# Performance work log

Measured on AMD Instinct MI355X. Metric: run time of the kernel, lower is better.

Reference implementation:

```python
import jax, jax.numpy as jnp
import numpy as np

B, S, D_IN, D_OUT = 4, 2048, 4096, 4096


def setup_inputs() -> dict:
    key = jax.random.key(0)
    k1, k2 = jax.random.split(key)
    x = jax.random.normal(k1, (B, S, D_IN), dtype=jnp.float32)
    # kaiming-uniform-like init scale; exact distribution irrelevant for correctness
    bound = 1.0 / np.sqrt(D_IN)
    weight = jax.random.uniform(k2, (D_OUT, D_IN), dtype=jnp.float32,
                                minval=-bound, maxval=bound)
    return {"x": x, "weight": weight}


def reference(x, weight):
    # absmean scale: gamma = mean(|W|)
    gamma = jnp.mean(jnp.abs(weight))
    # ternary quantize: round(W/gamma) clipped to {-1, 0, 1}; guard gamma==0
    safe_gamma = jnp.where(gamma == 0, 1.0, gamma)
    w_q = jnp.clip(jnp.round(weight / safe_gamma), -1.0, 1.0)
    w_q = jnp.where(gamma == 0, jnp.zeros_like(weight), w_q)
    # output = gamma * (x @ W_q^T)   (F.linear with no bias, scaled)
    out = jnp.einsum("bsd,od->bso", x, w_q) * gamma
    return out
```

## Files before the change

### kernel.cpp

```cpp
#include <hip/hip_runtime.h>
#include <hip/hip_bf16.h>
#include <stdint.h>

#define K_DIM 4096

typedef __attribute__((ext_vector_type(4))) float f32x4;
typedef __attribute__((ext_vector_type(4))) int i32x4;

#define GLOAD_LDS16(g, l)                                                        \
  __builtin_amdgcn_global_load_lds(                                              \
      (const __attribute__((address_space(1))) void*)(g),                        \
      (__attribute__((address_space(3))) void*)(l), 16, 0, 0)

__global__ void absum_partial(const float* __restrict__ W,
                              float* __restrict__ partials, int n) {
  int tid = blockIdx.x * blockDim.x + threadIdx.x;
  int stride = gridDim.x * blockDim.x;
  const f32x4* W4 = (const f32x4*)W;
  int n4 = n >> 2;
  float s = 0.f;
  for (int i = tid; i < n4; i += stride) {
    f32x4 v = W4[i];
    s += fabsf(v[0]) + fabsf(v[1]) + fabsf(v[2]) + fabsf(v[3]);
  }
#pragma unroll
  for (int off = 32; off > 0; off >>= 1) s += __shfl_down(s, off, 64);
  __shared__ float wsum[4];
  if ((threadIdx.x & 63) == 0) wsum[threadIdx.x >> 6] = s;
  __syncthreads();
  if (threadIdx.x == 0)
    partials[blockIdx.x] = wsum[0] + wsum[1] + wsum[2] + wsum[3];
}

__global__ void gamma_finalize(const float* __restrict__ partials,
                               float* __restrict__ gamma, float inv_n) {
  __shared__ float sm[256];
  int t = threadIdx.x;
  sm[t] = partials[t] + partials[t + 256] + partials[t + 512] + partials[t + 768];
  __syncthreads();
  for (int off = 128; off > 0; off >>= 1) {
    if (t < off) sm[t] += sm[t + off];
    __syncthreads();
  }
  if (t == 0) gamma[0] = sm[0] * inv_n;
}

__global__ void quantize_w_i8(const float* __restrict__ W,
                              signed char* __restrict__ Wq,
                              const float* __restrict__ gamma_p, int n) {
  float g = gamma_p[0];
  float safe = (g == 0.f) ? 1.f : g;
  int tid = blockIdx.x * blockDim.x + threadIdx.x;
  int stride = gridDim.x * blockDim.x;
  const f32x4* W4 = (const f32x4*)W;
  int n4 = n >> 2;
  int* out = (int*)Wq;
  for (int i = tid; i < n4; i += stride) {
    f32x4 v = W4[i];
    int b0, b1, b2, b3;
    float t0 = rintf(v[0] / safe);
    float t1 = rintf(v[1] / safe);
    float t2 = rintf(v[2] / safe);
    float t3 = rintf(v[3] / safe);
    b0 = (t0 >= 0.5f) ? 1 : (t0 <= -0.5f ? -1 : 0);
    b1 = (t1 >= 0.5f) ? 1 : (t1 <= -0.5f ? -1 : 0);
    b2 = (t2 >= 0.5f) ? 1 : (t2 <= -0.5f ? -1 : 0);
    b3 = (t3 >= 0.5f) ? 1 : (t3 <= -0.5f ? -1 : 0);
    out[i] = (b0 & 255) | ((b1 & 255) << 8) | ((b2 & 255) << 16) |
             ((b3 & 255) << 24);
  }
}

__global__ __launch_bounds__(256)
void quant_x_i8(const float* __restrict__ X, signed char* __restrict__ Xq,
                float* __restrict__ xscale) {
  int row = blockIdx.x;
  int t = threadIdx.x;
  const f32x4* xr = (const f32x4*)(X + (size_t)row * K_DIM);
  f32x4 v0 = xr[t], v1 = xr[t + 256], v2 = xr[t + 512], v3 = xr[t + 768];
  float mx = 0.f;
#define AMAX4(V)                                                               \
  mx = fmaxf(mx, fmaxf(fmaxf(fabsf(V[0]), fabsf(V[1])),                        \
                       fmaxf(fabsf(V[2]), fabsf(V[3]))));
  AMAX4(v0) AMAX4(v1) AMAX4(v2) AMAX4(v3)
#undef AMAX4
#pragma unroll
  for (int off = 32; off > 0; off >>= 1) mx = fmaxf(mx, __shfl_down(mx, off, 64));
  __shared__ float wmx[4];
  if ((t & 63) == 0) wmx[t >> 6] = mx;
  __syncthreads();
  float rmax = fmaxf(fmaxf(wmx[0], wmx[1]), fmaxf(wmx[2], wmx[3]));
  float inv = (rmax > 0.f) ? 127.0f / rmax : 0.f;
  if (t == 0) xscale[row] = (rmax > 0.f) ? rmax / 127.0f : 0.f;
  int* out = (int*)(Xq + (size_t)row * K_DIM);
#define PACK(V, IDX)                                                           \
  {                                                                            \
    int c0 = __float2int_rn(V[0] * inv), c1 = __float2int_rn(V[1] * inv);      \
    int c2 = __float2int_rn(V[2] * inv), c3 = __float2int_rn(V[3] * inv);      \
    out[IDX] = (c0 & 255) | ((c1 & 255) << 8) | ((c2 & 255) << 16) |           \
               ((c3 & 255) << 24);                                             \
  }
  PACK(v0, t) PACK(v1, t + 256) PACK(v2, t + 512) PACK(v3, t + 768)
#undef PACK
}

__global__ __launch_bounds__(512, 2)
void gemm256_i8(const signed char* __restrict__ A,
                const signed char* __restrict__ Bq,
                float* __restrict__ C,
                const float* __restrict__ gamma_p,
                const float* __restrict__ xscale, int M, int N) {
  __shared__ __align__(16) signed char Abuf[2][256][64];
  __shared__ __align__(16) signed char Bbuf[2][256][64];

  int ntN = N >> 8;
  int bid = blockIdx.x;
  int swz = (bid & 7) * (gridDim.x >> 3) + (bid >> 3);
  int tm = swz / ntN, tn = swz % ntN;

  int t = threadIdx.x;
  int lane = t & 63;
  int wid = t >> 6;
  int wr = wid >> 2, wc = wid & 3;
  int lr = lane & 15;
  int sc0 = (lane >> 4) ^ ((lr >> 1) & 3);

  const signed char* aG = A + (size_t)tm * 256 * K_DIM;
  const signed char* bG = Bq + (size_t)tn * 256 * K_DIM;

  int srow = t >> 2;
  int schunk = (t & 3) ^ ((t >> 3) & 3);
  const signed char* aSg = aG + (size_t)srow * K_DIM + (schunk << 4);
  const signed char* bSg = bG + (size_t)srow * K_DIM + (schunk << 4);
  char* aSl = (char*)Abuf + t * 16;
  char* bSl = (char*)Bbuf + t * 16;

  const signed char* aRd = &Abuf[0][0][0] + (wr * 128 + lr) * 64 + sc0 * 16;
  const signed char* bRd = &Bbuf[0][0][0] + (wc * 64 + lr) * 64 + sc0 * 16;

  i32x4 acc[8][4];
#pragma unroll
  for (int m = 0; m < 8; ++m)
#pragma unroll
    for (int n = 0; n < 4; ++n) acc[m][n] = (i32x4)(0);

#define STAGE_A(jj, S)                                                         \
  { GLOAD_LDS16(aSg + (size_t)(jj) * 64, aSl + (S) * 16384);                   \
    GLOAD_LDS16(aSg + (size_t)(jj) * 64 + (size_t)128 * K_DIM,                 \
                aSl + (S) * 16384 + 8192); }
#define STAGE_B(jj, S)                                                         \
  { GLOAD_LDS16(bSg + (size_t)(jj) * 64, bSl + (S) * 16384);                   \
    GLOAD_LDS16(bSg + (size_t)(jj) * 64 + (size_t)128 * K_DIM,                 \
                bSl + (S) * 16384 + 8192); }
#define BAR() __builtin_amdgcn_s_barrier()
#define VMC0() asm volatile("s_waitcnt vmcnt(0)" ::: "memory")
#define LGKM(NN) asm volatile("s_waitcnt lgkmcnt(" #NN ")" ::: "memory")
#define SB0() __builtin_amdgcn_sched_barrier(0)

#define TILE(S, JSTG, DO_STG, DO_END)                                          \
  {                                                                            \
    if (DO_STG) { STAGE_A(JSTG, (S) ^ 1); STAGE_B(JSTG, (S) ^ 1); }            \
    _Pragma("unroll") for (int n = 0; n < 4; ++n)                              \
      bfr[n] = *(const i32x4*)(bRd + (S) * 16384 + n * 1024);                  \
    _Pragma("unroll") for (int m = 0; m < 4; ++m)                              \
      at[m] = *(const i32x4*)(aRd + (S) * 16384 + m * 1024);                   \
    SB0();                                                                     \
    _Pragma("unroll") for (int m = 0; m < 4; ++m)                              \
      ab[m] = *(const i32x4*)(aRd + (S) * 16384 + 4096 + m * 1024);            \
    SB0();                                                                     \
    LGKM(4); SB0();                                                            \
    __builtin_amdgcn_s_setprio(1);                                             \
    _Pragma("unroll") for (int m = 0; m < 4; ++m)                              \
      _Pragma("unroll") for (int n = 0; n < 4; ++n)                            \
        acc[m][n] = __builtin_amdgcn_mfma_i32_16x16x64_i8(                     \
            at[m], bfr[n], acc[m][n], 0, 0, 0);                                \
    __builtin_amdgcn_s_setprio(0);                                             \
    LGKM(0); SB0();                                                            \
    __builtin_amdgcn_s_setprio(1);                                             \
    _Pragma("unroll") for (int m = 0; m < 4; ++m)                              \
      _Pragma("unroll") for (int n = 0; n < 4; ++n)                            \
        acc[4 + m][n] = __builtin_amdgcn_mfma_i32_16x16x64_i8(                 \
            ab[m], bfr[n], acc[4 + m][n], 0, 0, 0);                            \
    __builtin_amdgcn_s_setprio(0);                                             \
    if (DO_END) { VMC0(); BAR(); }                                             \
  }

  STAGE_A(0, 0); STAGE_B(0, 0);
  VMC0();
  BAR();

  i32x4 at[4], ab[4], bfr[4];
  for (int i = 0; i < 31; ++i) {
    int p = i << 1;
    TILE(0, p + 1, 1, 1);
    TILE(1, p + 2, 1, 1);
  }
  TILE(0, 63, 1, 1);
  TILE(1, 0, 0, 0);

  float g = gamma_p[0];
  int crow = (lane >> 4) << 2;
  size_t row0 = (size_t)tm * 256 + wr * 128 + crow;
  int col0 = tn * 256 + wc * 64 + lr;
#pragma unroll
  for (int m = 0; m < 8; ++m) {
#pragma unroll
    for (int j = 0; j < 4; ++j) {
      size_t row = row0 + m * 16 + j;
      float sc = g * xscale[row];
      float* cp = C + row * (size_t)N + col0;
#pragma unroll
      for (int n = 0; n < 4; ++n) cp[n * 16] = (float)acc[m][n][j] * sc;
    }
  }
#undef STAGE_A
#undef STAGE_B
#undef BAR
#undef VMC0
#undef LGKM
#undef SB0
#undef TILE
}

__global__ void naive_bitlinear(const float* __restrict__ X,
                                const float* __restrict__ W,
                                float* __restrict__ out,
                                const float* __restrict__ gamma_p, int M, int N) {
  int col = blockIdx.x * blockDim.x + threadIdx.x;
  int row = blockIdx.y;
  if (col >= N || row >= M) return;
  float g = gamma_p[0];
  float safe = (g == 0.f) ? 1.f : g;
  const float* x = X + (size_t)row * K_DIM;
  const float* w = W + (size_t)col * K_DIM;
  float s = 0.f;
  for (int k = 0; k < K_DIM; ++k) {
    float qv = fminf(fmaxf(rintf(w[k] / safe), -1.f), 1.f);
    s += x[k] * qv;
  }
  out[(size_t)row * N + col] = s * g;
}

extern "C" void kernel_launch(void* const* d_in, const int* in_sizes, int n_in,
                              void* d_out, int out_size, void* d_ws,
                              size_t ws_size, hipStream_t stream) {
  const float* x = (const float*)d_in[0];
  const float* w = (const float*)d_in[1];
  float* out = (float*)d_out;
  int xn = in_sizes[0];
  int wn = in_sizes[1];
  int M = xn / K_DIM;
  int N = wn / K_DIM;

  char* ws = (char*)d_ws;
  float* partials = (float*)ws;
  float* gamma = (float*)(ws + 4096);
  float* xscale = (float*)(ws + 8192);
  signed char* Wq = (signed char*)(ws + 8192 + 32768);
  signed char* Xq = Wq + (size_t)wn;
  size_t need = 8192 + 32768 + (size_t)wn + (size_t)xn;

  absum_partial<<<1024, 256, 0, stream>>>(w, partials, wn);
  gamma_finalize<<<1, 256, 0, stream>>>(partials, gamma, 1.0f / (float)wn);

  if (ws_size >= need && (M & 255) == 0 && (N & 255) == 0) {
    quantize_w_i8<<<2048, 256, 0, stream>>>(w, Wq, gamma, wn);
    quant_x_i8<<<M, 256, 0, stream>>>(x, Xq, xscale);
    int nwg = (M >> 8) * (N >> 8);
    gemm256_i8<<<nwg, 512, 0, stream>>>(Xq, Wq, out, gamma, xscale, M, N);
  } else {
    dim3 grid((N + 255) / 256, M);
    naive_bitlinear<<<grid, 256, 0, stream>>>(x, w, out, gamma, M, N);
  }
}
```

Baseline: 205.7 us.

## Restructure int8 GEMM main loop into 128-wide K tiles with finer staged prefetch

The int8 GEMM now uses 128-wide K tiles split into two 64-wide halves, doubling LDS to 128 KB per block. Each tile is processed in four phases that interleave LDS reads, MFMA groups and global-to-LDS prefetch of the next tiles, with partial vmcnt waits instead of full drains. The goal is better overlap of memory traffic with MFMA work and fewer full vmcnt(0) stalls. The cost is many more barriers per tile, and 128 KB of LDS per block may cut occupancy below the launch-bounds target of 2 blocks.

```diff
diff --git a/kernel.cpp b/kernel.cpp
--- a/kernel.cpp
+++ b/kernel.cpp
@@ -3,6 +3,7 @@
 #include <stdint.h>
 
 #define K_DIM 4096
+#define NKT   (K_DIM / 128)
 
 typedef __attribute__((ext_vector_type(4))) float f32x4;
 typedef __attribute__((ext_vector_type(4))) int i32x4;
@@ -105,13 +106,13 @@
 }
 
 __global__ __launch_bounds__(512, 2)
-void gemm256_i8(const signed char* __restrict__ A,
-                const signed char* __restrict__ Bq,
-                float* __restrict__ C,
-                const float* __restrict__ gamma_p,
-                const float* __restrict__ xscale, int M, int N) {
-  __shared__ __align__(16) signed char Abuf[2][256][64];
-  __shared__ __align__(16) signed char Bbuf[2][256][64];
+void gemm_i8_t(const signed char* __restrict__ A,
+               const signed char* __restrict__ Bq,
+               float* __restrict__ C,
+               const float* __restrict__ gamma_p,
+               const float* __restrict__ xscale, int M, int N) {
+  __shared__ __align__(16) signed char Ab[2][2][256][64];
+  __shared__ __align__(16) signed char Bb[2][2][256][64];
 
   int ntN = N >> 8;
   int bid = blockIdx.x;
@@ -123,20 +124,20 @@
   int wid = t >> 6;
   int wr = wid >> 2, wc = wid & 3;
   int lr = lane & 15;
-  int sc0 = (lane >> 4) ^ ((lr >> 1) & 3);
+  int cphys = (lane >> 4) ^ ((lr >> 1) & 3);
 
   const signed char* aG = A + (size_t)tm * 256 * K_DIM;
   const signed char* bG = Bq + (size_t)tn * 256 * K_DIM;
 
   int srow = t >> 2;
-  int schunk = (t & 3) ^ ((t >> 3) & 3);
-  const signed char* aSg = aG + (size_t)srow * K_DIM + (schunk << 4);
-  const signed char* bSg = bG + (size_t)srow * K_DIM + (schunk << 4);
-  char* aSl = (char*)Abuf + t * 16;
-  char* bSl = (char*)Bbuf + t * 16;
-
-  const signed char* aRd = &Abuf[0][0][0] + (wr * 128 + lr) * 64 + sc0 * 16;
-  const signed char* bRd = &Bbuf[0][0][0] + (wc * 64 + lr) * 64 + sc0 * 16;
+  int sclog = (t & 3) ^ ((t >> 3) & 3);
+  const signed char* aSg = aG + (size_t)srow * K_DIM + (sclog << 4);
+  const signed char* bSg = bG + (size_t)srow * K_DIM + (sclog << 4);
+  char* aSl = (char*)Ab + t * 16;
+  char* bSl = (char*)Bb + t * 16;
+
+  const signed char* aRd = &Ab[0][0][0][0] + (wr * 128 + lr) * 64 + cphys * 16;
+  const signed char* bRd = &Bb[0][0][0][0] + (wc * 64 + lr) * 64 + cphys * 16;
 
   i32x4 acc[8][4];
 #pragma unroll
@@ -144,59 +145,77 @@
 #pragma unroll
     for (int n = 0; n < 4; ++n) acc[m][n] = (i32x4)(0);
 
-#define STAGE_A(jj, S)                                                         \
-  { GLOAD_LDS16(aSg + (size_t)(jj) * 64, aSl + (S) * 16384);                   \
-    GLOAD_LDS16(aSg + (size_t)(jj) * 64 + (size_t)128 * K_DIM,                 \
-                aSl + (S) * 16384 + 8192); }
-#define STAGE_B(jj, S)                                                         \
-  { GLOAD_LDS16(bSg + (size_t)(jj) * 64, bSl + (S) * 16384);                   \
-    GLOAD_LDS16(bSg + (size_t)(jj) * 64 + (size_t)128 * K_DIM,                 \
-                bSl + (S) * 16384 + 8192); }
+#define STAGE_A(J, BUF, KS)                                                    \
+  { GLOAD_LDS16(aSg + (size_t)(J) * 128 + (KS) * 64,                           \
+                aSl + (BUF) * 32768 + (KS) * 16384);                           \
+    GLOAD_LDS16(aSg + (size_t)(J) * 128 + (KS) * 64 + (size_t)128 * K_DIM,     \
+                aSl + (BUF) * 32768 + (KS) * 16384 + 8192); }
+#define STAGE_B(J, BUF, KS)                                                    \
+  { GLOAD_LDS16(bSg + (size_t)(J) * 128 + (KS) * 64,                           \
+                bSl + (BUF) * 32768 + (KS) * 16384);                           \
+    GLOAD_LDS16(bSg + (size_t)(J) * 128 + (KS) * 64 + (size_t)128 * K_DIM,     \
+                bSl + (BUF) * 32768 + (KS) * 16384 + 8192); }
 #define BAR() __builtin_amdgcn_s_barrier()
-#define VMC0() asm volatile("s_waitcnt vmcnt(0)" ::: "memory")
-#define LGKM(NN) asm volatile("s_waitcnt lgkmcnt(" #NN ")" ::: "memory")
+#define VMC(NN) asm volatile("s_waitcnt vmcnt(" #NN ")" ::: "memory")
+#define LGKM0() asm volatile("s_waitcnt lgkmcnt(0)" ::: "memory")
 #define SB0() __builtin_amdgcn_sched_barrier(0)
-
-#define TILE(S, JSTG, DO_STG, DO_END)                                          \
-  {                                                                            \
-    if (DO_STG) { STAGE_A(JSTG, (S) ^ 1); STAGE_B(JSTG, (S) ^ 1); }            \
-    _Pragma("unroll") for (int n = 0; n < 4; ++n)                              \
-      bfr[n] = *(const i32x4*)(bRd + (S) * 16384 + n * 1024);                  \
-    _Pragma("unroll") for (int m = 0; m < 4; ++m)                              \
-      at[m] = *(const i32x4*)(aRd + (S) * 16384 + m * 1024);                   \
-    SB0();                                                                     \
-    _Pragma("unroll") for (int m = 0; m < 4; ++m)                              \
-      ab[m] = *(const i32x4*)(aRd + (S) * 16384 + 4096 + m * 1024);            \
-    SB0();                                                                     \
-    LGKM(4); SB0();                                                            \
-    __builtin_amdgcn_s_setprio(1);                                             \
+#define RD_B(BUF, KS)                                                          \
+  { _Pragma("unroll") for (int n = 0; n < 4; ++n)                              \
+      bfr[n] = *(const i32x4*)(bRd + (BUF) * 32768 + (KS) * 16384 + n * 1024); }
+#define RD_A(BUF, KS, MH)                                                      \
+  { _Pragma("unroll") for (int m = 0; m < 4; ++m)                              \
+      af[m] = *(const i32x4*)(aRd + (BUF) * 32768 + (KS) * 16384 +             \
+                              (MH) * 4096 + m * 1024); }
+#define MFMA16(MH)                                                             \
+  { __builtin_amdgcn_s_setprio(1);                                             \
     _Pragma("unroll") for (int m = 0; m < 4; ++m)                              \
       _Pragma("unroll") for (int n = 0; n < 4; ++n)                            \
-        acc[m][n] = __builtin_amdgcn_mfma_i32_16x16x64_i8(                     \
-            at[m], bfr[n], acc[m][n], 0, 0, 0);                                \
-    __builtin_amdgcn_s_setprio(0);                                             \
-    LGKM(0); SB0();                                                            \
-    __builtin_amdgcn_s_setprio(1);                                             \
-    _Pragma("unroll") for (int m = 0; m < 4; ++m)                              \
-      _Pragma("unroll") for (int n = 0; n < 4; ++n)                            \
-        acc[4 + m][n] = __builtin_amdgcn_mfma_i32_16x16x64_i8(                 \
-            ab[m], bfr[n], acc[4 + m][n], 0, 0, 0);                            \
-    __builtin_amdgcn_s_setprio(0);                                             \
-    if (DO_END) { VMC0(); BAR(); }                                             \
-  }
-
-  STAGE_A(0, 0); STAGE_B(0, 0);
-  VMC0();
+        acc[(MH) * 4 + m][n] = __builtin_amdgcn_mfma_i32_16x16x64_i8(          \
+            af[m], bfr[n], acc[(MH) * 4 + m][n], 0, 0, 0);                     \
+    __builtin_amdgcn_s_setprio(0); }
+
+#define TILE(KT, BUF, DO_S1, DO_S2, VEND)                                      \
+  {                                                                            \
+                                                   \
+    RD_B(BUF, 0); RD_A(BUF, 0, 0);                                             \
+    if (DO_S1) STAGE_A((KT) + 1, (BUF) ^ 1, 1);                                \
+    BAR(); LGKM0(); SB0();                                                     \
+    MFMA16(0);                                                                 \
+    BAR();                                                                     \
+                                                \
+    RD_A(BUF, 0, 1);                                                           \
+    if (DO_S2) STAGE_B((KT) + 2, BUF, 0);                                      \
+    BAR(); LGKM0(); SB0();                                                     \
+    MFMA16(1);                                                                 \
+    BAR();                                                                     \
+                                                   \
+    RD_B(BUF, 1); RD_A(BUF, 1, 0);                                             \
+    if (DO_S2) STAGE_A((KT) + 2, BUF, 0);                                      \
+    BAR(); LGKM0(); SB0();                                                     \
+    MFMA16(0);                                                                 \
+    BAR();                                                                     \
+                                          \
+    RD_A(BUF, 1, 1);                                                           \
+    if (DO_S2) STAGE_B((KT) + 2, BUF, 1);                                      \
+    BAR(); LGKM0(); SB0();                                                     \
+    MFMA16(1);                                                                 \
+    VEND; SB0();                                                               \
+    BAR();                                                                     \
+  }
+
+  STAGE_B(0, 0, 0); STAGE_A(0, 0, 0); STAGE_B(0, 0, 1); STAGE_A(0, 0, 1);
+  STAGE_B(1, 1, 0); STAGE_A(1, 1, 0); STAGE_B(1, 1, 1);
+  VMC(6); SB0();
   BAR();
 
-  i32x4 at[4], ab[4], bfr[4];
-  for (int i = 0; i < 31; ++i) {
-    int p = i << 1;
-    TILE(0, p + 1, 1, 1);
-    TILE(1, p + 2, 1, 1);
-  }
-  TILE(0, 63, 1, 1);
-  TILE(1, 0, 0, 0);
+  i32x4 af[4], bfr[4];
+  for (int i = 0; i < 15; ++i) {
+    int kt = i << 1;
+    TILE(kt, 0, 1, 1, VMC(6));
+    TILE(kt + 1, 1, 1, 1, VMC(6));
+  }
+  TILE(30, 0, 1, 0, VMC(0));
+  TILE(31, 1, 0, 0, (void)0);
 
   float g = gamma_p[0];
   int crow = (lane >> 4) << 2;
@@ -216,9 +235,12 @@
 #undef STAGE_A
 #undef STAGE_B
 #undef BAR
-#undef VMC0
-#undef LGKM
+#undef VMC
+#undef LGKM0
 #undef SB0
+#undef RD_B
+#undef RD_A
+#undef MFMA16
 #undef TILE
 }
 
@@ -267,7 +289,7 @@
     quantize_w_i8<<<2048, 256, 0, stream>>>(w, Wq, gamma, wn);
     quant_x_i8<<<M, 256, 0, stream>>>(x, Xq, xscale);
     int nwg = (M >> 8) * (N >> 8);
-    gemm256_i8<<<nwg, 512, 0, stream>>>(Xq, Wq, out, gamma, xscale, M, N);
+    gemm_i8_t<<<nwg, 512, 0, stream>>>(Xq, Wq, out, gamma, xscale, M, N);
   } else {
     dim3 grid((N + 255) / 256, M);
     naive_bitlinear<<<grid, 256, 0, stream>>>(x, w, out, gamma, M, N);
```

New measurement: 196.8 us. 4.3% less time.
